# Kernel optimization log

Measured on AMD Instinct MI355X. Metric: run time of the kernel, lower is better.

Reference implementation:

```python
import jax, jax.numpy as jnp
import numpy as np

N, C_IN, H, W = 32, 16, 256, 256
C_OUT, K = 64, 3

def setup_inputs() -> dict:
    key = jax.random.key(0)
    kx, kw, kb = jax.random.split(key, 3)
    x = jax.random.normal(kx, (N, C_IN, H, W), dtype=jnp.float32)
    # PyTorch Conv2d default init: U(-b, b), b = 1/sqrt(fan_in)
    bound = 1.0 / np.sqrt(C_IN * K * K)
    conv_weight = jax.random.uniform(kw, (C_OUT, C_IN, K, K), minval=-bound, maxval=bound, dtype=jnp.float32)
    conv_bias = jax.random.uniform(kb, (C_OUT,), minval=-bound, maxval=bound, dtype=jnp.float32)
    return {"x": x, "conv_weight": conv_weight, "conv_bias": conv_bias}

def reference(x, conv_weight, conv_bias):
    # conv2d, stride=1, padding=0 (VALID), NCHW / OIHW
    y = jax.lax.conv_general_dilated(
        x, conv_weight,
        window_strides=(1, 1), padding="VALID",
        dimension_numbers=("NCHW", "OIHW", "NCHW"))
    y = y + conv_bias[None, :, None, None]
    # min over output channels (keepdim -> 1 channel), then double tanh
    y = jnp.min(y, axis=1, keepdims=True)  # [N,1,OH,OW]
    return jnp.tanh(jnp.tanh(y))
```

## Files before the change

### kernel.cpp

```cpp
#include <hip/hip_runtime.h>

typedef __bf16 bf16x8 __attribute__((ext_vector_type(8)));
typedef unsigned short us8 __attribute__((ext_vector_type(8)));
typedef unsigned short us2 __attribute__((ext_vector_type(2)));
typedef float f32x16 __attribute__((ext_vector_type(16)));

#define N_IMG 32
#define CI 16
#define HH 256
#define WW 256
#define CO 64
#define OHH 254
#define OWW 254

#define XS_W 258
#define SC 24
#define NSTRIP 24
#define WP_SHORTS (CO * 160)
#define WS_NEEDED ((size_t)WP_SHORTS * 2)

__device__ __forceinline__ unsigned short f2bf(float f) {
  union { float f; unsigned u; } v; v.f = f;
  return (unsigned short)((v.u + 0x7FFFu + ((v.u >> 16) & 1u)) >> 16);
}

#if defined(__has_builtin)
#if __has_builtin(__builtin_amdgcn_cvt_pk_bf16_f32)
#define HAVE_CVT_PK 1
#endif
#endif

__device__ __forceinline__ us2 cvt2(float a, float b) {
#ifdef HAVE_CVT_PK
  typedef __bf16 bf16x2 __attribute__((ext_vector_type(2)));
  bf16x2 r = __builtin_amdgcn_cvt_pk_bf16_f32(a, b);
  return __builtin_bit_cast(us2, r);
#else
  us2 r; r[0] = f2bf(a); r[1] = f2bf(b); return r;
#endif
}

__device__ __forceinline__ float fast_tanh(float x) {
  float cx = fminf(fmaxf(x, -15.f), 15.f);
  float e = __expf(2.f * cx);
  return (e - 1.f) / (e + 1.f);
}

__device__ __forceinline__ void barrier_lds_only() {
  asm volatile("s_waitcnt lgkmcnt(0)" ::: "memory");
  __builtin_amdgcn_s_barrier();
  __builtin_amdgcn_sched_barrier(0);
}

__global__ void prep_w(const float* __restrict__ wg, const float* __restrict__ bg,
                       unsigned short* __restrict__ wp) {
  int idx = blockIdx.x * 256 + threadIdx.x;
  if (idx >= WP_SHORTS) return;
  int oc = idx / 160;
  int k = idx - oc * 160;
  int tap = k >> 4, ci = k & 15;
  float v;
  if (tap < 9)      v = wg[oc * 144 + ci * 9 + tap];
  else if (ci == 0) v = bg[oc];
  else              v = 0.f;
  wp[idx] = f2bf(v);
}

__global__ __launch_bounds__(256, 3)
void conv_fused(const float* __restrict__ xg, const unsigned short* __restrict__ wp,
                float* __restrict__ out) {
  __shared__ __align__(16) unsigned short xs[4 * XS_W * SC];
  const int t = threadIdx.x;
  const int n = blockIdx.x / NSTRIP;
  const int s = blockIdx.x - n * NSTRIP;
  const int oh0 = s * 10 + (s < 14 ? s : 14);
  const int nrows = (s < 14) ? 11 : 10;
  const int oh1 = oh0 + nrows;

  const float* srcT = xg + (size_t)n * (CI * HH * WW) + t;

  {
    float v[3][16];
#pragma unroll
    for (int r = 0; r < 3; ++r)
#pragma unroll
      for (int j = 0; j < 16; ++j)
        v[r][j] = srcT[((size_t)j * HH + (oh0 + r)) * WW];
#pragma unroll
    for (int r = 0; r < 3; ++r) {
      union { us8 v8[2]; us2 v2[8]; } pk;
#pragma unroll
      for (int j = 0; j < 8; ++j) pk.v2[j] = cvt2(v[r][2 * j], v[r][2 * j + 1]);
      const int slot = (oh0 + r) & 3;
      *(us8*)(xs + (slot * XS_W + t) * SC) = pk.v8[0];
      *(us8*)(xs + (slot * XS_W + t) * SC + 8) = pk.v8[1];
    }
  }
  if (t < 128) {
    const int slot = t >> 5, rem = t & 31;
    xs[(slot * XS_W + 256 + (rem >> 4)) * SC + (rem & 15)] = 0;
  }

  const int lane = t & 63, wave = t >> 6;
  const int lr = lane & 31, qh = lane >> 5;

  const unsigned short* wpl = wp + lr * 160 + qh * 8;
  bf16x8 afrag[2][10];
#pragma unroll
  for (int mt = 0; mt < 2; ++mt)
#pragma unroll
    for (int tap = 0; tap < 10; ++tap)
      afrag[mt][tap] =
          __builtin_bit_cast(bf16x8, *(const us8*)(wpl + mt * 32 * 160 + tap * 16));

  us8 onev = {};
  if (qh == 0) onev[0] = 0x3F80;
  const bf16x8 xone = __builtin_bit_cast(bf16x8, onev);

  const int pb = wave * 64;

  barrier_lds_only();

  for (int oh = oh0; oh < oh1; ++oh) {
    const bool do_stage = (oh + 1 < oh1);

    float v[16];
    if (do_stage) {
#pragma unroll
      for (int j = 0; j < 16; ++j)
        v[j] = srcT[((size_t)j * HH + (oh + 3)) * WW];
    }

    float vmin[2];
#pragma unroll
    for (int nt = 0; nt < 2; ++nt) {
      f32x16 acc0, acc1;
#pragma unroll
      for (int e = 0; e < 16; ++e) { acc0[e] = 0.f; acc1[e] = 0.f; }
#pragma unroll
      for (int tap = 0; tap < 9; ++tap) {
        const int kh = tap / 3, kw = tap - kh * 3;
        const int slot = (oh + kh) & 3;
        bf16x8 xf = __builtin_bit_cast(
            bf16x8,
            *(const us8*)(xs + (slot * XS_W + pb + nt * 32 + lr + kw) * SC + qh * 8));
        acc0 = __builtin_amdgcn_mfma_f32_32x32x16_bf16(afrag[0][tap], xf, acc0, 0, 0, 0);
        acc1 = __builtin_amdgcn_mfma_f32_32x32x16_bf16(afrag[1][tap], xf, acc1, 0, 0, 0);
      }
      acc0 = __builtin_amdgcn_mfma_f32_32x32x16_bf16(afrag[0][9], xone, acc0, 0, 0, 0);
      acc1 = __builtin_amdgcn_mfma_f32_32x32x16_bf16(afrag[1][9], xone, acc1, 0, 0, 0);

      f32x16 m;
#pragma unroll
      for (int e = 0; e < 16; ++e) m[e] = fminf(acc0[e], acc1[e]);
#pragma unroll
      for (int e = 0; e < 8; ++e) m[e] = fminf(m[e], m[e + 8]);
#pragma unroll
      for (int e = 0; e < 4; ++e) m[e] = fminf(m[e], m[e + 4]);
      float mv = fminf(fminf(m[0], m[1]), fminf(m[2], m[3]));
      mv = fminf(mv, __shfl_xor(mv, 32, 64));
      vmin[nt] = fast_tanh(fast_tanh(mv));
    }

    if (do_stage) {
      union { us8 v8[2]; us2 v2[8]; } pk;
#pragma unroll
      for (int j = 0; j < 8; ++j) pk.v2[j] = cvt2(v[2 * j], v[2 * j + 1]);
      const int slot = (oh + 3) & 3;
      *(us8*)(xs + (slot * XS_W + t) * SC) = pk.v8[0];
      *(us8*)(xs + (slot * XS_W + t) * SC + 8) = pk.v8[1];
    }

    const float res = (lane < 32) ? vmin[0] : vmin[1];
    const int ow = pb + lane;
    if (ow < OWW) out[((size_t)n * OHH + oh) * OWW + ow] = res;

    barrier_lds_only();
  }
}

#define XS_C 24
#define WS_K 168
__global__ __launch_bounds__(256, 2)
void conv_min_tanh(const float* __restrict__ xg, const float* __restrict__ wg,
                   const float* __restrict__ bg, float* __restrict__ out) {
  __shared__ __align__(16) unsigned short xs[3 * XS_W * XS_C];
  __shared__ __align__(16) unsigned short ws[CO * WS_K];
  const int t = threadIdx.x;
  const int n = blockIdx.x / OHH;
  const int oh = blockIdx.x % OHH;
#pragma unroll
  for (int i = 0; i < 36; ++i) {
    int f = i * 256 + t;
    int oc = f / 144;
    int r = f - oc * 144;
    int ci = r / 9;
    int tap = r - ci * 9;
    ws[oc * WS_K + tap * 16 + ci] = f2bf(wg[f]);
  }
  if (t < CO) ws[t * WS_K + 144] = f2bf(bg[t]);
  for (int i = t; i < CO * 15; i += 256) {
    int oc = i / 15;
    ws[oc * WS_K + 145 + (i - oc * 15)] = 0;
  }
  {
    const size_t base_n = (size_t)n * CI * HH * WW;
#pragma unroll
    for (int kh = 0; kh < 3; ++kh) {
#pragma unroll
      for (int half = 0; half < 2; ++half) {
        float v[8];
#pragma unroll
        for (int j = 0; j < 8; ++j) {
          int ci = half * 8 + j;
          v[j] = xg[base_n + ((size_t)ci * HH + (oh + kh)) * WW + t];
        }
        us8 pk;
#pragma unroll
        for (int j = 0; j < 8; ++j) pk[j] = f2bf(v[j]);
        *(us8*)(xs + (kh * XS_W + t) * XS_C + half * 8) = pk;
      }
    }
  }
  if (t < 96) {
    int kh = t >> 5;
    int rem = t & 31;
    int w = 256 + (rem >> 4);
    int ci = rem & 15;
    xs[(kh * XS_W + w) * XS_C + ci] = 0;
  }
  __syncthreads();
  const int lane = t & 63, wave = t >> 6;
  const int lr = lane & 31, qh = lane >> 5;
  bf16x8 afrag[2][10];
#pragma unroll
  for (int mt = 0; mt < 2; ++mt) {
    const unsigned short* wq = ws + (mt * 32 + lr) * WS_K + qh * 8;
#pragma unroll
    for (int tap = 0; tap < 10; ++tap)
      afrag[mt][tap] = __builtin_bit_cast(bf16x8, *(const us8*)(wq + tap * 16));
  }
  f32x16 acc[2][2];
#pragma unroll
  for (int a = 0; a < 2; ++a)
#pragma unroll
    for (int b = 0; b < 2; ++b)
#pragma unroll
      for (int e = 0; e < 16; ++e) acc[a][b][e] = 0.f;
  const unsigned short* xq = xs + (wave * 64 + lr) * XS_C + qh * 8;
#pragma unroll
  for (int tap = 0; tap < 9; ++tap) {
    const int kh = tap / 3, kw = tap - kh * 3;
#pragma unroll
    for (int nt = 0; nt < 2; ++nt) {
      bf16x8 xf = __builtin_bit_cast(
          bf16x8, *(const us8*)(xq + (kh * XS_W + nt * 32 + kw) * XS_C));
      acc[0][nt] = __builtin_amdgcn_mfma_f32_32x32x16_bf16(afrag[0][tap], xf,
                                                           acc[0][nt], 0, 0, 0);
      acc[1][nt] = __builtin_amdgcn_mfma_f32_32x32x16_bf16(afrag[1][tap], xf,
                                                           acc[1][nt], 0, 0, 0);
    }
  }
  {
    us8 one = {};
    if (qh == 0) one[0] = 0x3F80;
    bf16x8 xone = __builtin_bit_cast(bf16x8, one);
#pragma unroll
    for (int nt = 0; nt < 2; ++nt) {
      acc[0][nt] = __builtin_amdgcn_mfma_f32_32x32x16_bf16(afrag[0][9], xone,
                                                           acc[0][nt], 0, 0, 0);
      acc[1][nt] = __builtin_amdgcn_mfma_f32_32x32x16_bf16(afrag[1][9], xone,
                                                           acc[1][nt], 0, 0, 0);
    }
  }
  float vmin[2];
#pragma unroll
  for (int nt = 0; nt < 2; ++nt) {
    float v = acc[0][nt][0];
#pragma unroll
    for (int e = 1; e < 16; ++e) v = fminf(v, acc[0][nt][e]);
#pragma unroll
    for (int e = 0; e < 16; ++e) v = fminf(v, acc[1][nt][e]);
    v = fminf(v, __shfl_xor(v, 32, 64));
    vmin[nt] = fast_tanh(fast_tanh(v));
  }
  float res = (lane < 32) ? vmin[0] : vmin[1];
  int ow = wave * 64 + lane;
  if (ow < OWW) out[((size_t)n * OHH + oh) * OWW + ow] = res;
}

extern "C" void kernel_launch(void* const* d_in, const int* in_sizes, int n_in,
                              void* d_out, int out_size, void* d_ws, size_t ws_size,
                              hipStream_t stream) {
  const float* x = (const float*)d_in[0];
  const float* w = (const float*)d_in[1];
  const float* b = (const float*)d_in[2];
  float* out = (float*)d_out;
  if (ws_size >= WS_NEEDED) {
    unsigned short* wp = (unsigned short*)d_ws;
    prep_w<<<dim3((WP_SHORTS + 255) / 256), dim3(256), 0, stream>>>(w, b, wp);
    conv_fused<<<dim3(N_IMG * NSTRIP), dim3(256), 0, stream>>>(x, wp, out);
  } else {
    conv_min_tanh<<<dim3(N_IMG * OHH), dim3(256), 0, stream>>>(x, w, b, out);
  }
}
```

Measured before the change: 211.2 us.

## Process two output rows per iteration with a six-slot LDS ring buffer

The fused conv kernel now computes two output rows per loop iteration and stages two new input rows per step, using a 6-slot LDS ring instead of 4. This halves the number of block barriers and doubles the global load batch in flight. The LDS cell stride drops from 24 to 16 shorts, which reduces LDS use but may add bank conflicts on the strided fragment reads. Strip partitioning changes to 12/10 rows so every strip has an even row count. The custom lgkmcnt-only barrier is replaced by __syncthreads.

Result: slower. 218.0 us (+3.2%).

```diff
diff --git a/kernel.cpp b/kernel.cpp
--- a/kernel.cpp
+++ b/kernel.cpp
@@ -13,8 +13,9 @@
 #define OHH 254
 #define OWW 254
 
+#define SC 16
+#define SLOTS 6
 #define XS_W 258
-#define SC 24
 #define NSTRIP 24
 #define WP_SHORTS (CO * 160)
 #define WS_NEEDED ((size_t)WP_SHORTS * 2)
@@ -44,12 +45,6 @@
   float cx = fminf(fmaxf(x, -15.f), 15.f);
   float e = __expf(2.f * cx);
   return (e - 1.f) / (e + 1.f);
-}
-
-__device__ __forceinline__ void barrier_lds_only() {
-  asm volatile("s_waitcnt lgkmcnt(0)" ::: "memory");
-  __builtin_amdgcn_s_barrier();
-  __builtin_amdgcn_sched_barrier(0);
 }
 
 __global__ void prep_w(const float* __restrict__ wg, const float* __restrict__ bg,
@@ -69,36 +64,38 @@
 __global__ __launch_bounds__(256, 3)
 void conv_fused(const float* __restrict__ xg, const unsigned short* __restrict__ wp,
                 float* __restrict__ out) {
-  __shared__ __align__(16) unsigned short xs[4 * XS_W * SC];
+  __shared__ __align__(16) unsigned short xs[SLOTS * XS_W * SC];
   const int t = threadIdx.x;
   const int n = blockIdx.x / NSTRIP;
   const int s = blockIdx.x - n * NSTRIP;
-  const int oh0 = s * 10 + (s < 14 ? s : 14);
-  const int nrows = (s < 14) ? 11 : 10;
+  const int oh0 = (s < 7) ? 12 * s : 84 + 10 * (s - 7);
+  const int nrows = (s < 7) ? 12 : 10;
   const int oh1 = oh0 + nrows;
 
   const float* srcT = xg + (size_t)n * (CI * HH * WW) + t;
 
-  {
-    float v[3][16];
-#pragma unroll
-    for (int r = 0; r < 3; ++r)
-#pragma unroll
-      for (int j = 0; j < 16; ++j)
-        v[r][j] = srcT[((size_t)j * HH + (oh0 + r)) * WW];
-#pragma unroll
-    for (int r = 0; r < 3; ++r) {
-      union { us8 v8[2]; us2 v2[8]; } pk;
-#pragma unroll
-      for (int j = 0; j < 8; ++j) pk.v2[j] = cvt2(v[r][2 * j], v[r][2 * j + 1]);
-      const int slot = (oh0 + r) & 3;
-      *(us8*)(xs + (slot * XS_W + t) * SC) = pk.v8[0];
-      *(us8*)(xs + (slot * XS_W + t) * SC + 8) = pk.v8[1];
-    }
-  }
-  if (t < 128) {
+  if (t < 32 * SLOTS) {
     const int slot = t >> 5, rem = t & 31;
     xs[(slot * XS_W + 256 + (rem >> 4)) * SC + (rem & 15)] = 0;
+  }
+
+#pragma unroll
+  for (int b = 0; b < 2; ++b) {
+    float v[2][16];
+#pragma unroll
+    for (int r = 0; r < 2; ++r)
+#pragma unroll
+      for (int j = 0; j < 16; ++j)
+        v[r][j] = srcT[((size_t)j * HH + (oh0 + 2 * b + r)) * WW];
+#pragma unroll
+    for (int r = 0; r < 2; ++r) {
+      union { us8 v8[2]; us2 v2[8]; } pk;
+#pragma unroll
+      for (int j = 0; j < 8; ++j) pk.v2[j] = cvt2(v[r][2 * j], v[r][2 * j + 1]);
+      unsigned short* cell = xs + ((2 * b + r) * XS_W + t) * SC;
+      *(us8*)(cell) = pk.v8[0];
+      *(us8*)(cell + 8) = pk.v8[1];
+    }
   }
 
   const int lane = t & 63, wave = t >> 6;
@@ -119,63 +116,90 @@
 
   const int pb = wave * 64;
 
-  barrier_lds_only();
-
-  for (int oh = oh0; oh < oh1; ++oh) {
-    const bool do_stage = (oh + 1 < oh1);
-
-    float v[16];
+  __syncthreads();
+
+  int sb = 0;
+  for (int oh = oh0; oh < oh1; oh += 2) {
+    const bool do_stage = (oh + 4 <= oh1 + 1);
+
+    float v4[16], v5[16];
     if (do_stage) {
 #pragma unroll
       for (int j = 0; j < 16; ++j)
-        v[j] = srcT[((size_t)j * HH + (oh + 3)) * WW];
-    }
-
-    float vmin[2];
-#pragma unroll
-    for (int nt = 0; nt < 2; ++nt) {
-      f32x16 acc0, acc1;
-#pragma unroll
-      for (int e = 0; e < 16; ++e) { acc0[e] = 0.f; acc1[e] = 0.f; }
-#pragma unroll
-      for (int tap = 0; tap < 9; ++tap) {
-        const int kh = tap / 3, kw = tap - kh * 3;
-        const int slot = (oh + kh) & 3;
-        bf16x8 xf = __builtin_bit_cast(
-            bf16x8,
-            *(const us8*)(xs + (slot * XS_W + pb + nt * 32 + lr + kw) * SC + qh * 8));
-        acc0 = __builtin_amdgcn_mfma_f32_32x32x16_bf16(afrag[0][tap], xf, acc0, 0, 0, 0);
-        acc1 = __builtin_amdgcn_mfma_f32_32x32x16_bf16(afrag[1][tap], xf, acc1, 0, 0, 0);
+        v4[j] = srcT[((size_t)j * HH + (oh + 4)) * WW];
+#pragma unroll
+      for (int j = 0; j < 16; ++j)
+        v5[j] = srcT[((size_t)j * HH + (oh + 5)) * WW];
+    }
+
+    int so[4];
+#pragma unroll
+    for (int kh = 0; kh < 4; ++kh) {
+      int sl = sb + kh;
+      if (sl >= SLOTS) sl -= SLOTS;
+      so[kh] = sl * (XS_W * SC);
+    }
+
+#pragma unroll
+    for (int r2 = 0; r2 < 2; ++r2) {
+      float vmin[2];
+#pragma unroll
+      for (int nt = 0; nt < 2; ++nt) {
+        f32x16 acc0, acc1;
+#pragma unroll
+        for (int e = 0; e < 16; ++e) { acc0[e] = 0.f; acc1[e] = 0.f; }
+#pragma unroll
+        for (int tap = 0; tap < 9; ++tap) {
+          const int kh = tap / 3, kw = tap - kh * 3;
+          bf16x8 xf = __builtin_bit_cast(
+              bf16x8, *(const us8*)(xs + so[r2 + kh] +
+                                    (pb + nt * 32 + lr + kw) * SC + qh * 8));
+          acc0 = __builtin_amdgcn_mfma_f32_32x32x16_bf16(afrag[0][tap], xf, acc0, 0, 0, 0);
+          acc1 = __builtin_amdgcn_mfma_f32_32x32x16_bf16(afrag[1][tap], xf, acc1, 0, 0, 0);
+        }
+        acc0 = __builtin_amdgcn_mfma_f32_32x32x16_bf16(afrag[0][9], xone, acc0, 0, 0, 0);
+        acc1 = __builtin_amdgcn_mfma_f32_32x32x16_bf16(afrag[1][9], xone, acc1, 0, 0, 0);
+
+        f32x16 m;
+#pragma unroll
+        for (int e = 0; e < 16; ++e) m[e] = fminf(acc0[e], acc1[e]);
+#pragma unroll
+        for (int e = 0; e < 8; ++e) m[e] = fminf(m[e], m[e + 8]);
+#pragma unroll
+        for (int e = 0; e < 4; ++e) m[e] = fminf(m[e], m[e + 4]);
+        float mv = fminf(fminf(m[0], m[1]), fminf(m[2], m[3]));
+        mv = fminf(mv, __shfl_xor(mv, 32, 64));
+        vmin[nt] = fast_tanh(fast_tanh(mv));
       }
-      acc0 = __builtin_amdgcn_mfma_f32_32x32x16_bf16(afrag[0][9], xone, acc0, 0, 0, 0);
-      acc1 = __builtin_amdgcn_mfma_f32_32x32x16_bf16(afrag[1][9], xone, acc1, 0, 0, 0);
-
-      f32x16 m;
-#pragma unroll
-      for (int e = 0; e < 16; ++e) m[e] = fminf(acc0[e], acc1[e]);
-#pragma unroll
-      for (int e = 0; e < 8; ++e) m[e] = fminf(m[e], m[e + 8]);
-#pragma unroll
-      for (int e = 0; e < 4; ++e) m[e] = fminf(m[e], m[e + 4]);
-      float mv = fminf(fminf(m[0], m[1]), fminf(m[2], m[3]));
-      mv = fminf(mv, __shfl_xor(mv, 32, 64));
-      vmin[nt] = fast_tanh(fast_tanh(mv));
+      const float res = (lane < 32) ? vmin[0] : vmin[1];
+      const int ow = pb + lane;
+      if (ow < OWW) out[((size_t)n * OHH + (oh + r2)) * OWW + ow] = res;
     }
 
     if (do_stage) {
-      union { us8 v8[2]; us2 v2[8]; } pk;
-#pragma unroll
-      for (int j = 0; j < 8; ++j) pk.v2[j] = cvt2(v[2 * j], v[2 * j + 1]);
-      const int slot = (oh + 3) & 3;
-      *(us8*)(xs + (slot * XS_W + t) * SC) = pk.v8[0];
-      *(us8*)(xs + (slot * XS_W + t) * SC + 8) = pk.v8[1];
-    }
-
-    const float res = (lane < 32) ? vmin[0] : vmin[1];
-    const int ow = pb + lane;
-    if (ow < OWW) out[((size_t)n * OHH + oh) * OWW + ow] = res;
-
-    barrier_lds_only();
+      int s4 = sb + 4; if (s4 >= SLOTS) s4 -= SLOTS;
+      int s5 = sb + 5; if (s5 >= SLOTS) s5 -= SLOTS;
+      {
+        union { us8 v8[2]; us2 v2[8]; } pk;
+#pragma unroll
+        for (int j = 0; j < 8; ++j) pk.v2[j] = cvt2(v4[2 * j], v4[2 * j + 1]);
+        unsigned short* cell = xs + (s4 * XS_W + t) * SC;
+        *(us8*)(cell) = pk.v8[0];
+        *(us8*)(cell + 8) = pk.v8[1];
+      }
+      {
+        union { us8 v8[2]; us2 v2[8]; } pk;
+#pragma unroll
+        for (int j = 0; j < 8; ++j) pk.v2[j] = cvt2(v5[2 * j], v5[2 * j + 1]);
+        unsigned short* cell = xs + (s5 * XS_W + t) * SC;
+        *(us8*)(cell) = pk.v8[0];
+        *(us8*)(cell + 8) = pk.v8[1];
+      }
+    }
+
+    __syncthreads();
+    sb += 2;
+    if (sb >= SLOTS) sb -= SLOTS;
   }
 }
 
```
